# Kernel optimization log

Measured on AMD Instinct MI355X. Metric: run time of the kernel, lower is better.

The kernel has to match this reference:

```python
import jax, jax.numpy as jnp
import numpy as np
import math

FACTOR = 5

def setup_inputs() -> dict:
    key = jax.random.key(0)
    k1, k2, k3, k4 = jax.random.split(key, 4)
    B, L, H, D = 2, 4096, 8, 64
    sample_k = min(FACTOR * int(np.ceil(np.log(L))), L)  # 45
    return {
        "queries": jax.random.normal(k1, (B, L, H, D), dtype=jnp.float32),
        "keys": jax.random.normal(k2, (B, L, H, D), dtype=jnp.float32),
        "values": jax.random.normal(k3, (B, L, H, D), dtype=jnp.float32),
        "attn_mask": jnp.zeros((1,), dtype=bool),  # unused (mask_flag=False)
        "index_sample": jax.random.randint(k4, (L, sample_k), 0, L, dtype=jnp.int64),
    }

def reference(queries, keys, values, attn_mask, index_sample):
    B, L_Q, H, D = queries.shape
    L_K = keys.shape[1]
    # [B,L,H,D] -> [B,H,L,D]
    q = jnp.transpose(queries, (0, 2, 1, 3))
    k = jnp.transpose(keys, (0, 2, 1, 3))
    v = jnp.transpose(values, (0, 2, 1, 3))

    n_top = min(FACTOR * int(np.ceil(np.log(L_Q))), L_Q)  # u

    # --- _prob_QK ---
    # K_sample[b,h,l,s,e] = k[b,h,index_sample[l,s],e]
    K_sample = k[:, :, index_sample, :]                      # [B,H,L_Q,S,E]
    Q_K_sample = jnp.einsum('bhle,bhlse->bhls', q, K_sample)  # [B,H,L_Q,S]
    # sparsity measure: max - mean(over full L_K as in torch code)
    M = Q_K_sample.max(axis=-1) - Q_K_sample.sum(axis=-1) / L_K  # [B,H,L_Q]
    M_top = jax.lax.top_k(M, n_top)[1]                        # [B,H,u] indices

    Q_reduce = jnp.take_along_axis(q, M_top[..., None], axis=2)  # [B,H,u,E]
    scores_top = jnp.einsum('bhue,bhke->bhuk', Q_reduce, k)      # [B,H,u,L_K]

    scale = 1.0 / math.sqrt(D)
    attn = jax.nn.softmax(scale * scores_top, axis=-1)           # [B,H,u,L_K]
    context_in_q = jnp.einsum('bhuk,bhkd->bhud', attn, v)        # [B,H,u,D]

    # scatter selected contexts into zero-initialized tensor
    b_idx = jnp.arange(B)[:, None, None]
    h_idx = jnp.arange(H)[None, :, None]
    context = jnp.zeros((B, H, L_Q, D), dtype=queries.dtype)
    context = context.at[b_idx, h_idx, M_top].set(context_in_q)

    return jnp.transpose(context, (0, 2, 1, 3))  # [B,L_Q,H,D]
```

## Files before the change

kernel.cpp:

```cpp
#include <hip/hip_runtime.h>
#include <math.h>

#define B_ 2
#define L_ 4096
#define H_ 8
#define D_ 64
#define S_ 45
#define NTOP_ 45
#define SCALE 0.125f
#define TKEYS 64
#define NSPLIT 64

__global__ __launch_bounds__(256) void compute_M_kernel(
    const float* __restrict__ q, const float* __restrict__ k,
    const int* __restrict__ samp, float* __restrict__ M) {
    __shared__ int sIdx[32 * 49];
    int tid = threadIdx.x;
    int g   = blockIdx.x;
    int xcd = g & 7;
    int s0  = g >> 3;
    int bh  = xcd + 8 * (s0 >> 7);
    int c32 = s0 & 127;
    int b = bh >> 3, h = bh & 7;
    int l0 = c32 * 32;

    for (int i = tid; i < 32 * S_; i += 256) {
        int qq = i / S_, ss = i - qq * S_;
        sIdx[qq * 49 + ss] = samp[(long)(l0 + qq) * S_ + ss];
    }
    if (tid < 128) sIdx[(tid >> 2) * 49 + S_ + (tid & 3)] = 0;
    __syncthreads();

    int lane = tid & 63, wave = tid >> 6;
    int l8 = lane & 7;
    int q8 = lane >> 3;
    int qi = wave * 8 + q8;
    int l  = l0 + qi;

    const float4* qrow = (const float4*)(q + (((long)(b * L_ + l)) * H_ + h) * D_);
    float4 qa = qrow[l8], qb = qrow[8 + l8];

    const float4* kb4 = (const float4*)(k + ((long)b * L_ * H_ + h) * (long)D_);
    const int* myIdx = sIdx + qi * 49;

    const float4* r0 = kb4 + (long)myIdx[0] * (H_ * D_ / 4);
    float4 a0 = r0[l8], b0 = r0[8 + l8];
    const float4* r1 = kb4 + (long)myIdx[1] * (H_ * D_ / 4);
    float4 a1 = r1[l8], b1 = r1[8 + l8];
    const float4* r2 = kb4 + (long)myIdx[2] * (H_ * D_ / 4);
    float4 a2 = r2[l8], b2 = r2[8 + l8];

    float vmax = -INFINITY, vsum = 0.f;
    #pragma unroll 3
    for (int s = 0; s < S_; ++s) {
        int nidx = myIdx[s + 3];
        const float4* nr = kb4 + (long)nidx * (H_ * D_ / 4);
        float4 na = nr[l8], nb = nr[8 + l8];

        float p = qa.x * a0.x + qa.y * a0.y + qa.z * a0.z + qa.w * a0.w
                + qb.x * b0.x + qb.y * b0.y + qb.z * b0.z + qb.w * b0.w;
        p += __shfl_xor(p, 1, 64);
        p += __shfl_xor(p, 2, 64);
        p += __shfl_xor(p, 4, 64);
        vmax = fmaxf(vmax, p);
        vsum += p;

        a0 = a1; b0 = b1;
        a1 = a2; b1 = b2;
        a2 = na; b2 = nb;
    }
    if (l8 == 0)
        M[(long)bh * L_ + l] = vmax - vsum * (1.0f / (float)L_);
}

__global__ __launch_bounds__(256) void topk_kernel(
    const float* __restrict__ M, int* __restrict__ topIdx) {
    __shared__ unsigned int hist[256];
    __shared__ unsigned int suf[257];
    __shared__ unsigned int wsum[4];
    __shared__ int sBin, sRemain, sCnt, sTieCnt;
    __shared__ int tie[64];

    int bh = blockIdx.x, tid = threadIdx.x;
    int lane = tid & 63, wave = tid >> 6;
    const float* row = M + (long)bh * L_;

    unsigned int key[16];
    #pragma unroll
    for (int j = 0; j < 16; ++j) {
        unsigned int bts = __float_as_uint(row[tid + 256 * j]);
        key[j] = bts ^ ((unsigned int)((int)bts >> 31) | 0x80000000u);
    }

    unsigned int prefix = 0, pmask = 0;
    int remain = NTOP_;
    #pragma unroll 1
    for (int pass = 3; pass >= 0; --pass) {
        int shift = pass * 8;
        hist[tid] = 0;
        __syncthreads();
        #pragma unroll
        for (int j = 0; j < 16; ++j) {
            if ((key[j] & pmask) == prefix)
                atomicAdd(&hist[(key[j] >> shift) & 255u], 1u);
        }
        __syncthreads();
        unsigned int s = hist[tid];
        #pragma unroll
        for (int off = 1; off < 64; off <<= 1) {
            unsigned int o = __shfl_down(s, off, 64);
            if (lane + off < 64) s += o;
        }
        if (lane == 0) wsum[wave] = s;
        __syncthreads();
        unsigned int add = 0;
        for (int w = wave + 1; w < 4; ++w) add += wsum[w];
        s += add;
        suf[tid] = s;
        if (tid == 0) suf[256] = 0;
        __syncthreads();
        if (suf[tid] >= (unsigned int)remain && suf[tid + 1] < (unsigned int)remain) {
            sBin = tid;
            sRemain = remain - (int)suf[tid + 1];
        }
        __syncthreads();
        prefix |= ((unsigned int)sBin) << shift;
        pmask  |= 0xFFu << shift;
        remain  = sRemain;
        __syncthreads();
    }

    if (tid == 0) { sCnt = 0; sTieCnt = 0; }
    __syncthreads();
    int* outRow = topIdx + bh * NTOP_;
    #pragma unroll
    for (int j = 0; j < 16; ++j) {
        int idx = tid + 256 * j;
        if (key[j] > prefix) {
            int pos = atomicAdd(&sCnt, 1);
            outRow[pos] = idx;
        } else if (key[j] == prefix) {
            int tp = atomicAdd(&sTieCnt, 1);
            if (tp < 64) tie[tp] = idx;
        }
    }
    __syncthreads();
    if (tid == 0) {
        int base = sCnt;
        int tc = sTieCnt < 64 ? sTieCnt : 64;
        for (int t = 0; t < remain; ++t) {
            int mi = 0x7fffffff, mj = 0;
            for (int j2 = 0; j2 < tc; ++j2)
                if (tie[j2] < mi) { mi = tie[j2]; mj = j2; }
            outRow[base + t] = mi;
            tie[mj] = 0x7fffffff;
        }
    }
}

#define STRIDE 68
__global__ __launch_bounds__(256, 2) void attn_strip_kernel(
    const float* __restrict__ q, const float* __restrict__ k,
    const float* __restrict__ v, const int* __restrict__ topIdx,
    float* __restrict__ pOut, float* __restrict__ plPart, int nsplit) {
    __shared__ float sQ[48 * STRIDE];
    __shared__ float sK[TKEYS * STRIDE];
    __shared__ float sV[TKEYS * STRIDE];
    __shared__ float sP[48 * STRIDE];

    int g = blockIdx.x;
    int xcd = g & 7;
    int s0 = g >> 3;
    int grp = s0 / nsplit;
    int bh = xcd + 8 * grp;
    int split = s0 - grp * nsplit;
    int b = bh >> 3, h = bh & 7;
    int tid = threadIdx.x;
    int key0 = split * TKEYS;

    #pragma unroll
    for (int j = 0; j < 3; ++j) {
        int i = tid + 256 * j;
        int u = i >> 4, d4 = i & 15;
        float4 val = make_float4(0.f, 0.f, 0.f, 0.f);
        if (u < NTOP_) {
            int lq = topIdx[bh * NTOP_ + u];
            val = *(const float4*)(q + (((long)(b * L_ + lq)) * H_ + h) * D_ + 4 * d4);
        }
        *(float4*)(sQ + u * STRIDE + 4 * d4) = val;
    }
    #pragma unroll
    for (int j = 0; j < 4; ++j) {
        int i = tid + 256 * j;
        int r = i >> 4, d4 = i & 15;
        long off = (((long)(b * L_ + key0 + r)) * H_ + h) * D_ + 4 * d4;
        *(float4*)(sK + r * STRIDE + 4 * d4) = *(const float4*)(k + off);
        *(float4*)(sV + r * STRIDE + 4 * d4) = *(const float4*)(v + off);
    }
    __syncthreads();

    int tx = tid & 15, ty = tid >> 4;
    float acc[3][4];
    #pragma unroll
    for (int i = 0; i < 3; ++i)
        #pragma unroll
        for (int j = 0; j < 4; ++j) acc[i][j] = 0.f;

    #pragma unroll 4
    for (int d4 = 0; d4 < 16; ++d4) {
        float4 qv[3];
        #pragma unroll
        for (int i = 0; i < 3; ++i)
            qv[i] = *(const float4*)(sQ + (3 * ty + i) * STRIDE + 4 * d4);
        #pragma unroll
        for (int j = 0; j < 4; ++j) {
            float4 kv = *(const float4*)(sK + (tx + 16 * j) * STRIDE + 4 * d4);
            #pragma unroll
            for (int i = 0; i < 3; ++i)
                acc[i][j] += qv[i].x * kv.x + qv[i].y * kv.y + qv[i].z * kv.z + qv[i].w * kv.w;
        }
    }
    #pragma unroll
    for (int i = 0; i < 3; ++i) {
        #pragma unroll
        for (int j = 0; j < 4; ++j)
            sP[(3 * ty + i) * STRIDE + tx + 16 * j] = __expf(acc[i][j] * SCALE);
    }
    __syncthreads();

    int dx = tid & 15, uy = tid >> 4;
    float o[3][4];
    float ls[3];
    #pragma unroll
    for (int i = 0; i < 3; ++i) {
        ls[i] = 0.f;
        #pragma unroll
        for (int c = 0; c < 4; ++c) o[i][c] = 0.f;
    }
    #pragma unroll 4
    for (int k4 = 0; k4 < 16; ++k4) {
        float pa[3][4];
        #pragma unroll
        for (int i = 0; i < 3; ++i)
            *(float4*)pa[i] = *(const float4*)(sP + (3 * uy + i) * STRIDE + 4 * k4);
        #pragma unroll
        for (int c = 0; c < 4; ++c) {
            float4 vr = *(const float4*)(sV + (4 * k4 + c) * STRIDE + 4 * dx);
            #pragma unroll
            for (int i = 0; i < 3; ++i) {
                o[i][0] += pa[i][c] * vr.x;
                o[i][1] += pa[i][c] * vr.y;
                o[i][2] += pa[i][c] * vr.z;
                o[i][3] += pa[i][c] * vr.w;
                ls[i]   += pa[i][c];
            }
        }
    }
    #pragma unroll
    for (int i = 0; i < 3; ++i) {
        int u = 3 * uy + i;
        if (u < NTOP_) {
            long base = ((long)(split * 16 + bh) * NTOP_ + u) * D_;
            *(float4*)(pOut + base + 4 * dx) = make_float4(o[i][0], o[i][1], o[i][2], o[i][3]);
            if (dx == 0) plPart[(long)(split * 16 + bh) * NTOP_ + u] = ls[i];
        }
    }
}

__global__ __launch_bounds__(256) void reduce_norm_kernel(
    const int* __restrict__ topIdx, const float* __restrict__ pOut,
    const float* __restrict__ plPart, float* __restrict__ out, int nsplit) {
    __shared__ float part[4][64];
    __shared__ float lpart[4];
    int u = blockIdx.x, bh = blockIdx.y;
    int b = bh >> 3, h = bh & 7;
    int tid = threadIdx.x;
    int d = tid & 63, sg = tid >> 6;
    float acc = 0.f, lsum = 0.f;
    for (int s = sg; s < nsplit; s += 4) {
        acc  += pOut[((long)(s * 16 + bh) * NTOP_ + u) * D_ + d];
        lsum += plPart[(long)(s * 16 + bh) * NTOP_ + u];
    }
    part[sg][d] = acc;
    if (d == 0) lpart[sg] = lsum;
    __syncthreads();
    if (sg == 0) {
        float a = part[0][d] + part[1][d] + part[2][d] + part[3][d];
        float lt = lpart[0] + lpart[1] + lpart[2] + lpart[3];
        int lq = topIdx[bh * NTOP_ + u];
        out[(((long)(b * L_ + lq)) * H_ + h) * D_ + d] = a / lt;
    }
}

extern "C" void kernel_launch(void* const* d_in, const int* in_sizes, int n_in,
                              void* d_out, int out_size, void* d_ws, size_t ws_size,
                              hipStream_t stream) {
    const float* q = (const float*)d_in[0];
    const float* k = (const float*)d_in[1];
    const float* v = (const float*)d_in[2];
    const int* samp = (const int*)d_in[4];
    float* out = (float*)d_out;

    char* ws = (char*)d_ws;
    const size_t mBytes   = (size_t)B_ * H_ * L_ * sizeof(float);
    const size_t topBytes = (size_t)B_ * H_ * NTOP_ * sizeof(int);
    const size_t plBytes  = (size_t)NSPLIT * 16 * NTOP_ * sizeof(float);
    float* M      = (float*)ws;
    int*   topIdx = (int*)(ws + mBytes);
    float* plPart = (float*)(ws + mBytes + topBytes);
    float* pOut   = (float*)(ws + mBytes + topBytes + plBytes);

    int nsplit = NSPLIT;
    while (nsplit > 1) {
        size_t need = mBytes + topBytes + plBytes +
                      (size_t)nsplit * 16 * NTOP_ * D_ * sizeof(float);
        if (need <= ws_size) break;
        nsplit >>= 1;
    }

    hipMemsetAsync(d_out, 0, (size_t)out_size * sizeof(float), stream);

    compute_M_kernel<<<2048, 256, 0, stream>>>(q, k, samp, M);

    topk_kernel<<<B_ * H_, 256, 0, stream>>>(M, topIdx);

    attn_strip_kernel<<<nsplit * B_ * H_, 256, 0, stream>>>(
        q, k, v, topIdx, pOut, plPart, nsplit);

    dim3 gn(NTOP_, B_ * H_);
    reduce_norm_kernel<<<gn, 256, 0, stream>>>(topIdx, pOut, plPart, out, nsplit);
}
```

Before: 159.6 us.

## Fuse output zeroing with split reduction and scatter; remap compute_M to head pairs

The separate memset of the output is dropped. A new kernel zeroes each 32-row output tile, finds which rows are top-k selections through a shared-memory scan, and reduces and normalises the split partials for those rows. compute_M is remapped so each block covers 8 query rows across two adjacent heads, reading contiguous 512-byte K rows per gathered index, and the lane reduction uses DPP permutes in place of some shuffles. This trades a memset plus a reduce launch for one fused kernel, and makes the sampled-key gathers more coalesced, at the cost of per-thread linear searches over the top-k list.

```diff
diff --git a/kernel.cpp b/kernel.cpp
--- a/kernel.cpp
+++ b/kernel.cpp
@@ -11,66 +11,61 @@
 #define TKEYS 64
 #define NSPLIT 64
 
+template<int CTRL>
+__device__ __forceinline__ float dpp_permf(float x) {
+    return __int_as_float(__builtin_amdgcn_update_dpp(
+        0, __float_as_int(x), CTRL, 0xF, 0xF, true));
+}
+
 __global__ __launch_bounds__(256) void compute_M_kernel(
     const float* __restrict__ q, const float* __restrict__ k,
     const int* __restrict__ samp, float* __restrict__ M) {
-    __shared__ int sIdx[32 * 49];
+    __shared__ int sIdx[8 * 48];
     int tid = threadIdx.x;
     int g   = blockIdx.x;
     int xcd = g & 7;
-    int s0  = g >> 3;
-    int bh  = xcd + 8 * (s0 >> 7);
-    int c32 = s0 & 127;
-    int b = bh >> 3, h = bh & 7;
-    int l0 = c32 * 32;
-
-    for (int i = tid; i < 32 * S_; i += 256) {
+    int chunk = g >> 3;
+    int b  = xcd >> 2;
+    int h0 = (xcd & 3) * 2;
+    int l0 = chunk * 8;
+
+    for (int i = tid; i < 8 * S_; i += 256) {
         int qq = i / S_, ss = i - qq * S_;
-        sIdx[qq * 49 + ss] = samp[(long)(l0 + qq) * S_ + ss];
-    }
-    if (tid < 128) sIdx[(tid >> 2) * 49 + S_ + (tid & 3)] = 0;
+        sIdx[qq * 48 + ss] = samp[(long)(l0 + qq) * S_ + ss];
+    }
+    if (tid < 24) sIdx[(tid / 3) * 48 + S_ + (tid % 3)] = 0;
     __syncthreads();
 
     int lane = tid & 63, wave = tid >> 6;
-    int l8 = lane & 7;
-    int q8 = lane >> 3;
-    int qi = wave * 8 + q8;
-    int l  = l0 + qi;
-
-    const float4* qrow = (const float4*)(q + (((long)(b * L_ + l)) * H_ + h) * D_);
-    float4 qa = qrow[l8], qb = qrow[8 + l8];
-
-    const float4* kb4 = (const float4*)(k + ((long)b * L_ * H_ + h) * (long)D_);
-    const int* myIdx = sIdx + qi * 49;
-
-    const float4* r0 = kb4 + (long)myIdx[0] * (H_ * D_ / 4);
-    float4 a0 = r0[l8], b0 = r0[8 + l8];
-    const float4* r1 = kb4 + (long)myIdx[1] * (H_ * D_ / 4);
-    float4 a1 = r1[l8], b1 = r1[8 + l8];
-    const float4* r2 = kb4 + (long)myIdx[2] * (H_ * D_ / 4);
-    float4 a2 = r2[l8], b2 = r2[8 + l8];
+    int c  = lane & 31;
+    int q8 = wave * 2 + (lane >> 5);
+    int l  = l0 + q8;
+
+    float4 q4 = ((const float4*)(q + (((long)(b * L_ + l)) * H_ + h0) * D_))[c];
+    const float4* kb4 = (const float4*)(k + ((long)b * L_ * H_ + h0) * (long)D_);
+    const int* myIdx = sIdx + q8 * 48;
+
+    float4 f0 = kb4[(long)myIdx[0] * 128 + c];
+    float4 f1 = kb4[(long)myIdx[1] * 128 + c];
+    float4 f2 = kb4[(long)myIdx[2] * 128 + c];
 
     float vmax = -INFINITY, vsum = 0.f;
     #pragma unroll 3
     for (int s = 0; s < S_; ++s) {
-        int nidx = myIdx[s + 3];
-        const float4* nr = kb4 + (long)nidx * (H_ * D_ / 4);
-        float4 na = nr[l8], nb = nr[8 + l8];
-
-        float p = qa.x * a0.x + qa.y * a0.y + qa.z * a0.z + qa.w * a0.w
-                + qb.x * b0.x + qb.y * b0.y + qb.z * b0.z + qb.w * b0.w;
-        p += __shfl_xor(p, 1, 64);
-        p += __shfl_xor(p, 2, 64);
+        float4 nf = kb4[(long)myIdx[s + 3] * 128 + c];
+        float p = q4.x * f0.x + q4.y * f0.y + q4.z * f0.z + q4.w * f0.w;
+        p += dpp_permf<0xB1>(p);
+        p += dpp_permf<0x4E>(p);
         p += __shfl_xor(p, 4, 64);
+        p += __shfl_xor(p, 8, 64);
         vmax = fmaxf(vmax, p);
         vsum += p;
-
-        a0 = a1; b0 = b1;
-        a1 = a2; b1 = b2;
-        a2 = na; b2 = nb;
-    }
-    if (l8 == 0)
-        M[(long)bh * L_ + l] = vmax - vsum * (1.0f / (float)L_);
+        f0 = f1; f1 = f2; f2 = nf;
+    }
+    if ((lane & 15) == 0) {
+        int h = h0 + ((lane >> 4) & 1);
+        M[(long)(b * 8 + h) * L_ + l] = vmax - vsum * (1.0f / (float)L_);
+    }
 }
 
 __global__ __launch_bounds__(256) void topk_kernel(
@@ -267,28 +262,50 @@
     }
 }
 
-__global__ __launch_bounds__(256) void reduce_norm_kernel(
+__global__ __launch_bounds__(256) void zero_reduce_scatter_kernel(
     const int* __restrict__ topIdx, const float* __restrict__ pOut,
     const float* __restrict__ plPart, float* __restrict__ out, int nsplit) {
-    __shared__ float part[4][64];
-    __shared__ float lpart[4];
-    int u = blockIdx.x, bh = blockIdx.y;
-    int b = bh >> 3, h = bh & 7;
+    __shared__ int sTop[8 * NTOP_];
+    __shared__ int sel[256];
+    __shared__ int selCnt;
+    int g = blockIdx.x;
+    int b = g >> 7;
+    int l0 = (g & 127) * 32;
     int tid = threadIdx.x;
-    int d = tid & 63, sg = tid >> 6;
-    float acc = 0.f, lsum = 0.f;
-    for (int s = sg; s < nsplit; s += 4) {
-        acc  += pOut[((long)(s * 16 + bh) * NTOP_ + u) * D_ + d];
-        lsum += plPart[(long)(s * 16 + bh) * NTOP_ + u];
-    }
-    part[sg][d] = acc;
-    if (d == 0) lpart[sg] = lsum;
-    __syncthreads();
-    if (sg == 0) {
-        float a = part[0][d] + part[1][d] + part[2][d] + part[3][d];
-        float lt = lpart[0] + lpart[1] + lpart[2] + lpart[3];
-        int lq = topIdx[bh * NTOP_ + u];
-        out[(((long)(b * L_ + lq)) * H_ + h) * D_ + d] = a / lt;
+    if (tid == 0) selCnt = 0;
+    for (int i = tid; i < 8 * NTOP_; i += 256) sTop[i] = topIdx[b * 8 * NTOP_ + i];
+    __syncthreads();
+
+    float4* obase = (float4*)(out + ((long)(b * L_ + l0)) * H_ * D_);
+    float4 z = make_float4(0.f, 0.f, 0.f, 0.f);
+    #pragma unroll
+    for (int j = 0; j < 16; ++j) obase[tid + 256 * j] = z;
+
+    {
+        int l = l0 + (tid >> 3), h = tid & 7;
+        const int* rowp = sTop + h * NTOP_;
+        int u = -1;
+        #pragma unroll
+        for (int t = 0; t < NTOP_; ++t)
+            if (rowp[t] == l) u = t;
+        if (u >= 0) { int p = atomicAdd(&selCnt, 1); sel[p] = (tid << 8) | u; }
+    }
+    __syncthreads();
+
+    int lane = tid & 63, wave = tid >> 6;
+    int n = selCnt;
+    for (int w = wave; w < n; w += 4) {
+        int e = sel[w];
+        int t = e >> 8, u = e & 255;
+        int l = l0 + (t >> 3), h = t & 7, bh = b * 8 + h;
+        float lv = (lane < nsplit) ? plPart[((long)lane * 16 + bh) * NTOP_ + u] : 0.f;
+        #pragma unroll
+        for (int o = 32; o > 0; o >>= 1) lv += __shfl_xor(lv, o, 64);
+        float accv = 0.f;
+        const float* pb = pOut + ((long)bh * NTOP_ + u) * D_ + lane;
+        #pragma unroll 8
+        for (int s = 0; s < nsplit; ++s) accv += pb[(long)s * 16 * NTOP_ * D_];
+        out[(((long)(b * L_ + l)) * H_ + h) * D_ + lane] = accv / lv;
     }
 }
 
@@ -318,15 +335,13 @@
         nsplit >>= 1;
     }
 
-    hipMemsetAsync(d_out, 0, (size_t)out_size * sizeof(float), stream);
-
-    compute_M_kernel<<<2048, 256, 0, stream>>>(q, k, samp, M);
+    compute_M_kernel<<<4096, 256, 0, stream>>>(q, k, samp, M);
 
     topk_kernel<<<B_ * H_, 256, 0, stream>>>(M, topIdx);
 
     attn_strip_kernel<<<nsplit * B_ * H_, 256, 0, stream>>>(
         q, k, v, topIdx, pOut, plPart, nsplit);
 
-    dim3 gn(NTOP_, B_ * H_);
-    reduce_norm_kernel<<<gn, 256, 0, stream>>>(topIdx, pOut, plPart, out, nsplit);
-}
+    zero_reduce_scatter_kernel<<<B_ * (L_ / 32), 256, 0, stream>>>(
+        topIdx, pOut, plPart, out, nsplit);
+}
```

After: 163.5 us. 2.4% more time.
